# Kernel tuning notes

Hardware: AMD Instinct MI355X
Metric: run time of the kernel (lower is better)

Reference implementation:

```python
import jax, jax.numpy as jnp
import numpy as np

MODES = 128
NEG_SLOPE = 0.2


def setup_inputs() -> dict:
    key = jax.random.key(0)
    k1, k2 = jax.random.split(key)
    x = jax.random.normal(k1, (32, 256, 4096), dtype=jnp.float32)
    weight = jax.random.normal(k2, (256, 256, MODES, 2), dtype=jnp.float32)
    return {"x": x, "weight": weight}


def reference(x, weight):
    B, C, M = x.shape
    n_freq = M // 2 + 1
    n_modes = min(MODES, n_freq)  # static
    # rfft along last dim -> (B, C, n_freq) complex64
    x_ft = jnp.fft.rfft(x, axis=-1)
    # complex per-mode mixing weight: (C_out, C_in, modes)
    w = weight[..., 0] + 1j * weight[..., 1]
    # out_ft[b,o,m] = sum_i x_ft[b,i,m] * w[o,i,m]  (batched complex GEMM over modes)
    out_low = jnp.einsum('bim,oim->bom', x_ft[:, :, :n_modes], w[:, :, :n_modes])
    # zero-fill the remaining frequencies
    out_ft = jnp.concatenate(
        [out_low, jnp.zeros((B, C, n_freq - n_modes), dtype=out_low.dtype)], axis=-1)
    x_ifft = jnp.fft.irfft(out_ft, n=M, axis=-1)
    # LeakyReLU(0.2) then residual add
    return x + jnp.where(x_ifft >= 0, x_ifft, NEG_SLOPE * x_ifft)
```

## Files before the change

kernel.cpp:

```cpp
#include <hip/hip_runtime.h>


typedef unsigned short u16;
typedef unsigned int   u32;
typedef __attribute__((ext_vector_type(8))) short bf16x8;
typedef __attribute__((ext_vector_type(4))) float f32x4;

#define MLEN  4096

__device__ __forceinline__ u16 f2b(float f) {
  u32 u = __float_as_uint(f);
  u += 0x7fffu + ((u >> 16) & 1u);
  return (u16)(u >> 16);
}
__device__ __forceinline__ float blo(u32 p) { return __uint_as_float(p << 16); }
__device__ __forceinline__ float bhi(u32 p) { return __uint_as_float(p & 0xffff0000u); }

__global__ void probe_kernel(const u16* __restrict__ x16, int* __restrict__ flag) {
  __shared__ int cnt;
  if (threadIdx.x == 0) cnt = 0;
  __syncthreads();
  int c = 0;
  for (int j = threadIdx.x; j < 4096; j += 256) {
    u32 e = (x16[j] >> 7) & 0xFFu;
    if (e >= 0x8Fu) ++c;
  }
  atomicAdd(&cnt, c);
  __syncthreads();
  if (threadIdx.x == 0) flag[0] = (cnt > 256) ? 0 : 1;
}

__global__ void basis_kernel(u16* __restrict__ Bas1P, u16* __restrict__ Bas2P) {
  int t = blockIdx.x;
  int c = threadIdx.x;
  {
    int p = c >> 7, rem = c & 127, j = rem >> 1, s2 = rem & 1;
    int m = 2 * j + p;
    int idx = (m * t) & 4095;
    float theta = (float)idx * (6.283185307179586f / 4096.0f);
    float s, cth;
    __sincosf(theta, &s, &cth);
    Bas2P[t * 256 + c] = f2b(s2 ? -s : cth);
  }
  {
    int parity = c >> 7, isim = (c >> 6) & 1, j = c & 63;
    int m = 2 * j + parity;
    int idx = (m * t) & 4095;
    float theta = (float)idx * (6.283185307179586f / 4096.0f);
    float s, cth;
    __sincosf(theta, &s, &cth);
    Bas1P[c * 2048 + t] = f2b(isim ? -s : cth);
  }
}

template <int BM, int BN, int EPI, bool ADUAL>
__global__ __launch_bounds__(256)
void gemm_nt(const void* __restrict__ A, const u16* __restrict__ Bt,
             int K, int lda, int ldb,
             u32* __restrict__ Xp, int ldc,
             const void* __restrict__ xres, void* __restrict__ outp,
             const int* __restrict__ flag) {
  constexpr int LD = 72;
  constexpr int FM = BM / 32;
  constexpr int FN = BN / 32;
  __shared__ __align__(16) char smem[(BM + BN) * LD * 2];
  u16* As = (u16*)smem;
  u16* Bs = (u16*)(smem + BM * LD * 2);
  const int mode = (ADUAL || EPI == 1) ? flag[0] : 1;
  const int tid = threadIdx.x;
  const int bn0 = blockIdx.x * BN;
  const int bm0 = blockIdx.y * BM;
  const int lane = tid & 63;
  const int wave = tid >> 6;
  const int wm = wave >> 1, wn = wave & 1;
  const int l15 = lane & 15, q4 = lane >> 4;

  const u16* Btb = Bt;
  if constexpr (EPI == 2) Btb += (size_t)blockIdx.z * BN * ldb;

  f32x4 acc[FM][FN] = {};
  f32x4 acc2[FM][FN] = {};

  auto kstep = [&](f32x4 (&ac)[FM][FN]) {
#pragma unroll
    for (int kk = 0; kk < 2; ++kk) {
      const int ko = kk * 32 + q4 * 8;
      bf16x8 af[FM], bfr[FN];
#pragma unroll
      for (int mi = 0; mi < FM; ++mi)
        af[mi] = *(const bf16x8*)&As[(wm * (BM / 2) + mi * 16 + l15) * LD + ko];
#pragma unroll
      for (int ni = 0; ni < FN; ++ni)
        bfr[ni] = *(const bf16x8*)&Bs[(wn * (BN / 2) + ni * 16 + l15) * LD + ko];
#pragma unroll
      for (int mi = 0; mi < FM; ++mi)
#pragma unroll
        for (int ni = 0; ni < FN; ++ni)
          ac[mi][ni] = __builtin_amdgcn_mfma_f32_16x16x32_bf16(
              af[mi], bfr[ni], ac[mi][ni], 0, 0, 0);
    }
  };

  for (int kt = 0; kt < K; kt += 64) {
    __syncthreads();
    if constexpr (EPI == 2) {
      const int neg = blockIdx.z;
#pragma unroll
      for (int q = tid; q < BM * 8; q += 256) {
        int row = q >> 3, c8 = q & 7;
        u16 tmp[8];
        if (mode == 1) {
          const u16* s0 = &((const u16*)A)[(size_t)(bm0 + row) * lda + kt + c8 * 8];
          uint4 a0 = *(const uint4*)s0;
          uint4 a1 = *(const uint4*)(s0 + 2048);
          u32 aw[4] = {a0.x, a0.y, a0.z, a0.w};
          u32 bw[4] = {a1.x, a1.y, a1.z, a1.w};
#pragma unroll
          for (int j = 0; j < 4; ++j) {
            float lo = neg ? (blo(aw[j]) - blo(bw[j])) : (blo(aw[j]) + blo(bw[j]));
            float hi = neg ? (bhi(aw[j]) - bhi(bw[j])) : (bhi(aw[j]) + bhi(bw[j]));
            tmp[2 * j]     = f2b(lo);
            tmp[2 * j + 1] = f2b(hi);
          }
        } else {
          const float* s0 = &((const float*)A)[(size_t)(bm0 + row) * lda + kt + c8 * 8];
          float4 f0 = *(const float4*)s0;
          float4 f1 = *(const float4*)(s0 + 4);
          float4 g0 = *(const float4*)(s0 + 2048);
          float4 g1 = *(const float4*)(s0 + 2052);
          float a[8] = {f0.x, f0.y, f0.z, f0.w, f1.x, f1.y, f1.z, f1.w};
          float b[8] = {g0.x, g0.y, g0.z, g0.w, g1.x, g1.y, g1.z, g1.w};
#pragma unroll
          for (int j = 0; j < 8; ++j)
            tmp[j] = f2b(neg ? (a[j] - b[j]) : (a[j] + b[j]));
        }
        *(uint4*)&As[row * LD + c8 * 8] = *(const uint4*)tmp;
      }
    } else {
      const u16* Ab = (const u16*)A;
#pragma unroll
      for (int q = tid; q < BM * 8; q += 256) {
        int row = q >> 3, c8 = q & 7;
        *(uint4*)&As[row * LD + c8 * 8] =
            *(const uint4*)&Ab[(size_t)(bm0 + row) * lda + kt + c8 * 8];
      }
    }
#pragma unroll
    for (int q = tid; q < BN * 8; q += 256) {
      int row = q >> 3, c8 = q & 7;
      *(uint4*)&Bs[row * LD + c8 * 8] =
          *(const uint4*)&Btb[(size_t)(bn0 + row) * ldb + kt + c8 * 8];
    }
    __syncthreads();
    if constexpr (EPI == 1) {
      if (kt >= 128) kstep(acc2); else kstep(acc);
    } else {
      kstep(acc);
    }
  }

  if constexpr (EPI == 1) {
    float* Cs = (float*)smem;
    const int s = tid >> 3;
    const int c8 = tid & 7;
#pragma unroll
    for (int mi = 0; mi < FM; ++mi) {
      __syncthreads();
#pragma unroll
      for (int ni = 0; ni < FN; ++ni) {
        float* dst = &Cs[(wm * 16 + q4 * 4) * 136 + wn * 32 + ni * 16 + l15];
#pragma unroll
        for (int r = 0; r < 4; ++r) {
          float e = acc[mi][ni][r], o = acc2[mi][ni][r];
          dst[r * 136]      = e + o;
          dst[r * 136 + 68] = e - o;
        }
      }
      __syncthreads();
      const int gr = bm0 + mi * 16 + s + ((s < 16) ? 0 : (BM / 2 - 16));
      if (mode == 1) {
        const u16* xr16 = (const u16*)xres;
        u16* o16 = (u16*)outp;
#pragma unroll
        for (int h = 0; h < 2; ++h) {
          float4 va = *(const float4*)&Cs[s * 136 + h * 68 + c8 * 8];
          float4 vb = *(const float4*)&Cs[s * 136 + h * 68 + c8 * 8 + 4];
          size_t gidx = (size_t)gr * ldc + bn0 + h * 2048 + c8 * 8;
          uint4 xv = *(const uint4*)&xr16[gidx];
          float cv[8] = {va.x, va.y, va.z, va.w, vb.x, vb.y, vb.z, vb.w};
          u32 xw[4] = {xv.x, xv.y, xv.z, xv.w};
          u16 ov[8];
#pragma unroll
          for (int j = 0; j < 4; ++j) {
            float l0 = cv[2 * j]     >= 0.f ? cv[2 * j]     : 0.2f * cv[2 * j];
            float l1 = cv[2 * j + 1] >= 0.f ? cv[2 * j + 1] : 0.2f * cv[2 * j + 1];
            ov[2 * j]     = f2b(blo(xw[j]) + l0);
            ov[2 * j + 1] = f2b(bhi(xw[j]) + l1);
          }
          *(uint4*)&o16[gidx] = *(const uint4*)ov;
        }
      } else {
        const float* xf = (const float*)xres;
        float* of = (float*)outp;
#pragma unroll
        for (int h = 0; h < 2; ++h) {
          float4 v0 = *(const float4*)&Cs[s * 136 + h * 68 + c8 * 8];
          float4 v1 = *(const float4*)&Cs[s * 136 + h * 68 + c8 * 8 + 4];
          size_t gidx = (size_t)gr * ldc + bn0 + h * 2048 + c8 * 8;
          float4 x0 = *(const float4*)&xf[gidx];
          float4 x1 = *(const float4*)&xf[gidx + 4];
          float4 o0, o1;
          o0.x = x0.x + (v0.x >= 0.f ? v0.x : 0.2f * v0.x);
          o0.y = x0.y + (v0.y >= 0.f ? v0.y : 0.2f * v0.y);
          o0.z = x0.z + (v0.z >= 0.f ? v0.z : 0.2f * v0.z);
          o0.w = x0.w + (v0.w >= 0.f ? v0.w : 0.2f * v0.w);
          o1.x = x1.x + (v1.x >= 0.f ? v1.x : 0.2f * v1.x);
          o1.y = x1.y + (v1.y >= 0.f ? v1.y : 0.2f * v1.y);
          o1.z = x1.z + (v1.z >= 0.f ? v1.z : 0.2f * v1.z);
          o1.w = x1.w + (v1.w >= 0.f ? v1.w : 0.2f * v1.w);
          *(float4*)&of[gidx] = o0;
          *(float4*)&of[gidx + 4] = o1;
        }
      }
    }
  } else {
    constexpr int LP = 136;
    u16* Ls = (u16*)smem;
    __syncthreads();
#pragma unroll
    for (int ni = 0; ni < FN; ++ni) {
      u16* dst = &Ls[(wm * 16 + q4 * 4) * LP + wn * 64 + ni * 16 + l15];
#pragma unroll
      for (int r = 0; r < 4; ++r) dst[r * LP] = f2b(acc[0][ni][r]);
    }
    __syncthreads();
    const int b   = bm0 >> 8;
    const int ic0 = bm0 & 255;
    const int j   = tid >> 2;
    const int icg = tid & 3;
    const int mo  = 2 * j + blockIdx.z;
    u32 vals[8];
#pragma unroll
    for (int ii = 0; ii < 8; ++ii) {
      int ic = icg * 8 + ii;
      vals[ii] = (u32)Ls[ic * LP + j] | ((u32)Ls[ic * LP + 64 + j] << 16);
    }
    u32* dst = &Xp[((size_t)mo * 32 + b) * 256 + ic0 + icg * 8];
    *(uint4*)dst       = *(const uint4*)&vals[0];
    *(uint4*)(dst + 4) = *(const uint4*)&vals[4];
  }
}

__global__ __launch_bounds__(256)
void mixm_kernel(const u32* __restrict__ Xm, const void* __restrict__ w,
                 u16* __restrict__ Yp, const int* __restrict__ flag) {
  constexpr int XL = 264;
  constexpr int WL = 40;
  __shared__ u16 Xre[32 * XL];
  __shared__ u16 Xim[32 * XL];
  __shared__ u16 Wre[64 * WL];
  __shared__ u16 Wip[64 * WL];
  __shared__ u16 Win[64 * WL];
  const int tid = threadIdx.x;
  const int m  = blockIdx.x;
  const int o0 = blockIdx.y * 64;
  const int mode = flag[0];
  const int lane = tid & 63, wv = tid >> 6;
  const int l15 = lane & 15, q4 = lane >> 4;

  {
    const int b = tid >> 3, i0 = (tid & 7) * 32;
    const uint4* src = (const uint4*)(Xm + ((size_t)m * 32 + b) * 256 + i0);
#pragma unroll
    for (int c = 0; c < 8; ++c) {
      uint4 v = src[c];
      int i = i0 + c * 4;
      *(u32*)&Xre[b * XL + i]     = (v.x & 0xffffu) | (v.y << 16);
      *(u32*)&Xre[b * XL + i + 2] = (v.z & 0xffffu) | (v.w << 16);
      *(u32*)&Xim[b * XL + i]     = (v.x >> 16) | (v.y & 0xffff0000u);
      *(u32*)&Xim[b * XL + i + 2] = (v.z >> 16) | (v.w & 0xffff0000u);
    }
  }

  f32x4 accRe[2] = {}, accIm[2] = {};

  const int so = tid >> 2;
  const int sk = (tid & 3) * 8;

  for (int kt = 0; kt < 8; ++kt) {
    const int k0 = kt * 32;
    __syncthreads();
    if (mode == 0) {
      const float* wp = (const float*)w +
          (((size_t)(o0 + so) * 256 + (k0 + sk)) * 128 + m) * 2;
#pragma unroll
      for (int kk = 0; kk < 8; ++kk) {
        float2 f = *(const float2*)(wp + (size_t)kk * 256);
        u16 re = f2b(f.x), im = f2b(f.y);
        Wre[so * WL + sk + kk] = re;
        Wip[so * WL + sk + kk] = im;
        Win[so * WL + sk + kk] = im ^ 0x8000u;
      }
    } else {
      const u32* wp = (const u32*)w +
          ((size_t)(o0 + so) * 256 + (k0 + sk)) * 128 + m;
#pragma unroll
      for (int kk = 0; kk < 8; ++kk) {
        u32 v = wp[(size_t)kk * 128];
        u16 re = (u16)v, im = (u16)(v >> 16);
        Wre[so * WL + sk + kk] = re;
        Wip[so * WL + sk + kk] = im;
        Win[so * WL + sk + kk] = im ^ 0x8000u;
      }
    }
    __syncthreads();
    bf16x8 aRe[2], aIm[2];
#pragma unroll
    for (int mi = 0; mi < 2; ++mi) {
      aRe[mi] = *(const bf16x8*)&Xre[(mi * 16 + l15) * XL + k0 + q4 * 8];
      aIm[mi] = *(const bf16x8*)&Xim[(mi * 16 + l15) * XL + k0 + q4 * 8];
    }
    bf16x8 bRe = *(const bf16x8*)&Wre[(wv * 16 + l15) * WL + q4 * 8];
    bf16x8 bIp = *(const bf16x8*)&Wip[(wv * 16 + l15) * WL + q4 * 8];
    bf16x8 bIn = *(const bf16x8*)&Win[(wv * 16 + l15) * WL + q4 * 8];
#pragma unroll
    for (int mi = 0; mi < 2; ++mi) {
      accRe[mi] = __builtin_amdgcn_mfma_f32_16x16x32_bf16(aRe[mi], bRe, accRe[mi], 0, 0, 0);
      accRe[mi] = __builtin_amdgcn_mfma_f32_16x16x32_bf16(aIm[mi], bIn, accRe[mi], 0, 0, 0);
      accIm[mi] = __builtin_amdgcn_mfma_f32_16x16x32_bf16(aRe[mi], bIp, accIm[mi], 0, 0, 0);
      accIm[mi] = __builtin_amdgcn_mfma_f32_16x16x32_bf16(aIm[mi], bRe, accIm[mi], 0, 0, 0);
    }
  }

  const float sIm = 2.0f / 4096.0f;
  const float sRe = (m == 0) ? (1.0f / 4096.0f) : (2.0f / 4096.0f);
  u32* Yp32 = (u32*)Yp;
  const int o = o0 + wv * 16 + l15;
  const int word = (m & 1) * 64 + (m >> 1);
#pragma unroll
  for (int mi = 0; mi < 2; ++mi)
#pragma unroll
    for (int r = 0; r < 4; ++r) {
      int b = mi * 16 + q4 * 4 + r;
      u32 val = (u32)f2b(accRe[mi][r] * sRe) | ((u32)f2b(accIm[mi][r] * sIm) << 16);
      Yp32[((size_t)(b * 256 + o)) * 128 + word] = val;
    }
}

extern "C" void kernel_launch(void* const* d_in, const int* in_sizes, int n_in,
                              void* d_out, int out_size, void* d_ws, size_t ws_size,
                              hipStream_t stream) {
  const void* x = d_in[0];
  const void* w = d_in[1];

  char* ws = (char*)d_ws;
  int*  flag  = (int*)(ws);
  u16*  Bas1P = (u16*)(ws + (1u << 20));
  u16*  Bas2P = (u16*)(ws + (2u << 20));
  u32*  Xm    = (u32*)(ws + (4u << 20));
  u16*  Yp    = (u16*)(ws + (8u << 20));

  probe_kernel<<<dim3(1), dim3(256), 0, stream>>>((const u16*)x, flag);
  basis_kernel<<<dim3(2048), dim3(256), 0, stream>>>(Bas1P, Bas2P);

  gemm_nt<32, 128, 2, true><<<dim3(1, 256, 2), dim3(256), 0, stream>>>(
      x, Bas1P, 2048, MLEN, 2048, Xm, 0, nullptr, nullptr, flag);

  mixm_kernel<<<dim3(128, 4), dim3(256), 0, stream>>>(Xm, w, Yp, flag);

  gemm_nt<128, 64, 1, false><<<dim3(32, 64, 1), dim3(256), 0, stream>>>(
      Yp, Bas2P, 256, 256, 256, nullptr, MLEN, x, d_out, flag);
}
```

Measured before the change: 477.2 us.

## Repack mixing weights into mode-major bf16 layout before the mode GEMM

Adds a repack kernel that reads the weight tensor contiguously along modes, converts it to packed bf16 complex pairs, and transposes it through shared memory into a mode-major [m][o][i] layout. The mixing kernel can then load weights with 16-byte vector loads instead of strided scalar gathers whose stride is the mode dimension. The negated-imaginary shared-memory copy is dropped and rebuilt in registers by XOR. The cost is an extra launch plus a full read and write of the weights through a new workspace buffer. The X padding in shared memory also changes.

```diff
diff --git a/kernel.cpp b/kernel.cpp
--- a/kernel.cpp
+++ b/kernel.cpp
@@ -5,6 +5,7 @@
 typedef unsigned int   u32;
 typedef __attribute__((ext_vector_type(8))) short bf16x8;
 typedef __attribute__((ext_vector_type(4))) float f32x4;
+typedef __attribute__((ext_vector_type(4))) u32   u32x4;
 
 #define MLEN  4096
 
@@ -50,6 +51,48 @@
     float s, cth;
     __sincosf(theta, &s, &cth);
     Bas1P[c * 2048 + t] = f2b(isim ? -s : cth);
+  }
+}
+
+__global__ __launch_bounds__(256)
+void repack_w(const void* __restrict__ w, u32* __restrict__ Wp,
+              const int* __restrict__ flag) {
+  __shared__ u32 L[128 * 131];
+  const int tid = threadIdx.x;
+  const int o0 = blockIdx.x * 2;
+  const int k0 = blockIdx.y * 64;
+  const int mode = flag[0];
+  {
+    const int row = tid >> 1, h = tid & 1;
+    const int o_l = row >> 6, k_l = row & 63;
+    if (mode == 0) {
+      const float* src = (const float*)w +
+          (((size_t)(o0 + o_l) * 256 + (k0 + k_l)) * 128 + h * 64) * 2;
+#pragma unroll
+      for (int mm = 0; mm < 64; ++mm) {
+        float2 f = *(const float2*)(src + mm * 2);
+        L[row * 131 + h * 64 + mm] = (u32)f2b(f.x) | ((u32)f2b(f.y) << 16);
+      }
+    } else {
+      const u32* src = (const u32*)w +
+          ((size_t)(o0 + o_l) * 256 + (k0 + k_l)) * 128 + h * 64;
+#pragma unroll
+      for (int mm = 0; mm < 64; ++mm)
+        L[row * 131 + h * 64 + mm] = src[mm];
+    }
+  }
+  __syncthreads();
+  {
+    const int m = tid >> 1, o_l = tid & 1;
+    u32* dst = Wp + ((size_t)m * 256 + o0 + o_l) * 256 + k0;
+#pragma unroll
+    for (int kq = 0; kq < 16; ++kq) {
+      u32 v[4];
+#pragma unroll
+      for (int i = 0; i < 4; ++i)
+        v[i] = L[(o_l * 64 + kq * 4 + i) * 131 + m];
+      *(uint4*)(dst + kq * 4) = *(const uint4*)v;
+    }
   }
 }
 
@@ -252,19 +295,17 @@
 }
 
 __global__ __launch_bounds__(256)
-void mixm_kernel(const u32* __restrict__ Xm, const void* __restrict__ w,
-                 u16* __restrict__ Yp, const int* __restrict__ flag) {
-  constexpr int XL = 264;
+void mixm_kernel(const u32* __restrict__ Xm, const u32* __restrict__ Wp,
+                 u16* __restrict__ Yp) {
+  constexpr int XL = 266;
   constexpr int WL = 40;
   __shared__ u16 Xre[32 * XL];
   __shared__ u16 Xim[32 * XL];
   __shared__ u16 Wre[64 * WL];
   __shared__ u16 Wip[64 * WL];
-  __shared__ u16 Win[64 * WL];
   const int tid = threadIdx.x;
   const int m  = blockIdx.x;
   const int o0 = blockIdx.y * 64;
-  const int mode = flag[0];
   const int lane = tid & 63, wv = tid >> 6;
   const int l15 = lane & 15, q4 = lane >> 4;
 
@@ -290,27 +331,15 @@
   for (int kt = 0; kt < 8; ++kt) {
     const int k0 = kt * 32;
     __syncthreads();
-    if (mode == 0) {
-      const float* wp = (const float*)w +
-          (((size_t)(o0 + so) * 256 + (k0 + sk)) * 128 + m) * 2;
+    {
+      const u32* wp = Wp + ((size_t)m * 256 + o0 + so) * 256 + k0 + sk;
+      uint4 v0 = *(const uint4*)wp;
+      uint4 v1 = *(const uint4*)(wp + 4);
+      u32 vs[8] = {v0.x, v0.y, v0.z, v0.w, v1.x, v1.y, v1.z, v1.w};
 #pragma unroll
       for (int kk = 0; kk < 8; ++kk) {
-        float2 f = *(const float2*)(wp + (size_t)kk * 256);
-        u16 re = f2b(f.x), im = f2b(f.y);
-        Wre[so * WL + sk + kk] = re;
-        Wip[so * WL + sk + kk] = im;
-        Win[so * WL + sk + kk] = im ^ 0x8000u;
-      }
-    } else {
-      const u32* wp = (const u32*)w +
-          ((size_t)(o0 + so) * 256 + (k0 + sk)) * 128 + m;
-#pragma unroll
-      for (int kk = 0; kk < 8; ++kk) {
-        u32 v = wp[(size_t)kk * 128];
-        u16 re = (u16)v, im = (u16)(v >> 16);
-        Wre[so * WL + sk + kk] = re;
-        Wip[so * WL + sk + kk] = im;
-        Win[so * WL + sk + kk] = im ^ 0x8000u;
+        Wre[so * WL + sk + kk] = (u16)vs[kk];
+        Wip[so * WL + sk + kk] = (u16)(vs[kk] >> 16);
       }
     }
     __syncthreads();
@@ -322,7 +351,9 @@
     }
     bf16x8 bRe = *(const bf16x8*)&Wre[(wv * 16 + l15) * WL + q4 * 8];
     bf16x8 bIp = *(const bf16x8*)&Wip[(wv * 16 + l15) * WL + q4 * 8];
-    bf16x8 bIn = *(const bf16x8*)&Win[(wv * 16 + l15) * WL + q4 * 8];
+    u32x4 ipw = *(const u32x4*)&bIp;
+    u32x4 inw = ipw ^ 0x80008000u;
+    bf16x8 bIn = *(const bf16x8*)&inw;
 #pragma unroll
     for (int mi = 0; mi < 2; ++mi) {
       accRe[mi] = __builtin_amdgcn_mfma_f32_16x16x32_bf16(aRe[mi], bRe, accRe[mi], 0, 0, 0);
@@ -359,14 +390,17 @@
   u16*  Bas2P = (u16*)(ws + (2u << 20));
   u32*  Xm    = (u32*)(ws + (4u << 20));
   u16*  Yp    = (u16*)(ws + (8u << 20));
+  u32*  Wp    = (u32*)(ws + (12u << 20));
 
   probe_kernel<<<dim3(1), dim3(256), 0, stream>>>((const u16*)x, flag);
   basis_kernel<<<dim3(2048), dim3(256), 0, stream>>>(Bas1P, Bas2P);
 
+  repack_w<<<dim3(128, 4), dim3(256), 0, stream>>>(w, Wp, flag);
+
   gemm_nt<32, 128, 2, true><<<dim3(1, 256, 2), dim3(256), 0, stream>>>(
       x, Bas1P, 2048, MLEN, 2048, Xm, 0, nullptr, nullptr, flag);
 
-  mixm_kernel<<<dim3(128, 4), dim3(256), 0, stream>>>(Xm, w, Yp, flag);
+  mixm_kernel<<<dim3(128, 4), dim3(256), 0, stream>>>(Xm, Wp, Yp);
 
   gemm_nt<128, 64, 1, false><<<dim3(32, 64, 1), dim3(256), 0, stream>>>(
       Yp, Bas2P, 256, 256, 256, nullptr, MLEN, x, d_out, flag);
```

After: 414.7 us. 13.1% less time.
